# Optimization experiments

Hardware: AMD Instinct MI355X
Metric: run time of the kernel (lower is better)

Reference implementation:

```python
import jax, jax.numpy as jnp
import numpy as np

N_CLASSES = 80
SCORE_THRESH = 0.3
NMS_THRESH = 0.3
TOPK = 100            # max candidates kept per (image, class) for fixed-shape NMS
MAX_PER_IMAGE = 50
ANCHORS = np.array([[10,13],[16,30],[33,23],[30,61],[62,45],[59,119],
                    [116,90],[156,198],[373,326]], dtype=np.float32)
ANCHOR_MASK = ((6,7,8),(3,4,5),(0,1,2))


def setup_inputs() -> dict:
    key = jax.random.key(0)
    k0, k1, k2 = jax.random.split(key, 3)
    B = 16
    feat0 = jax.random.normal(k0, (B, 255, 19, 19), jnp.float32)
    feat1 = jax.random.normal(k1, (B, 255, 38, 38), jnp.float32)
    feat2 = jax.random.normal(k2, (B, 255, 76, 76), jnp.float32)
    anchors = jnp.asarray(ANCHORS)
    image_shape = jnp.array([480.0, 640.0], jnp.float32)  # (h, w) of original image
    return {"feat0": feat0, "feat1": feat1, "feat2": feat2,
            "anchors": anchors, "image_shape": image_shape}


def _decode_scale(feat, anchors_s, input_hw, image_shape):
    # feat: [B, 3*(5+C), gh, gw] -> boxes [B, gh*gw*3, 4], scores [B, gh*gw*3, C]
    B, _, gh, gw = feat.shape
    fm = feat.reshape(B, 3, 5 + N_CLASSES, gh, gw).transpose(0, 3, 4, 1, 2)  # [B,gh,gw,3,5+C]
    gy, gx = jnp.meshgrid(jnp.arange(gh, dtype=feat.dtype),
                          jnp.arange(gw, dtype=feat.dtype), indexing='ij')
    grid = jnp.stack([gx, gy], -1)[None, :, :, None, :]           # [1,gh,gw,1,2] (x,y)
    box_xy = (jax.nn.sigmoid(fm[..., :2]) + grid) / jnp.array([gh, gw], feat.dtype)
    box_wh = anchors_s[None, None, None, :, :] * jnp.exp(fm[..., 2:4]) / input_hw
    conf = jax.nn.sigmoid(fm[..., 4:5])
    probs = jax.nn.sigmoid(fm[..., 5:])
    # letterbox correction (keras-yolo3 yolo_correct_boxes)
    box_yx = box_xy[..., ::-1]
    box_hw = box_wh[..., ::-1]
    new_shape = jnp.round(image_shape * jnp.min(input_hw / image_shape))
    offset = (input_hw - new_shape) / 2.0 / input_hw
    scale = input_hw / new_shape
    box_yx = (box_yx - offset) * scale
    box_hw = box_hw * scale
    mins = box_yx - box_hw / 2.0
    maxes = box_yx + box_hw / 2.0
    boxes = jnp.concatenate([mins, maxes], -1) * jnp.concatenate([image_shape, image_shape])
    scores = conf * probs
    return boxes.reshape(B, -1, 4), scores.reshape(B, -1, N_CLASSES)


def _iou_matrix(b):  # b: [K,4] as (y1,x1,y2,x2)
    y1, x1, y2, x2 = b[:, 0], b[:, 1], b[:, 2], b[:, 3]
    area = (y2 - y1) * (x2 - x1)
    iy1 = jnp.maximum(y1[:, None], y1[None, :])
    ix1 = jnp.maximum(x1[:, None], x1[None, :])
    iy2 = jnp.minimum(y2[:, None], y2[None, :])
    ix2 = jnp.minimum(x2[:, None], x2[None, :])
    inter = jnp.maximum(iy2 - iy1, 0.0) * jnp.maximum(ix2 - ix1, 0.0)
    return inter / (area[:, None] + area[None, :] - inter + 1e-9)


def _nms_class(boxes, scores):  # boxes [N,4], scores [N] -> dets [TOPK,5] (zero-padded)
    s = jnp.where(scores > SCORE_THRESH, scores, -1.0)
    top_s, idx = jax.lax.top_k(s, TOPK)      # candidates sorted descending
    b = boxes[idx]                            # [TOPK,4]
    iou = _iou_matrix(b)
    valid = top_s > SCORE_THRESH
    ar = jnp.arange(TOPK)
    def body(i, keep):
        active = keep[i] & valid[i]
        sup = active & (iou[i] > NMS_THRESH) & (ar > i)
        return keep & ~sup
    keep = jax.lax.fori_loop(0, TOPK, body, valid)
    dets = jnp.concatenate([b, top_s[:, None]], -1)
    return dets * keep[:, None].astype(b.dtype)


def reference(feat0, feat1, feat2, anchors, image_shape):
    input_hw = jnp.array([feat0.shape[2] * 32, feat0.shape[3] * 32], feat0.dtype)
    boxes_all, scores_all = [], []
    for feat, mask in zip((feat0, feat1, feat2), ANCHOR_MASK):
        bx, sc = _decode_scale(feat, anchors[jnp.array(mask)], input_hw, image_shape)
        boxes_all.append(bx)
        scores_all.append(sc)
    boxes = jnp.concatenate(boxes_all, 1)    # [B,N,4]
    scores = jnp.concatenate(scores_all, 1)  # [B,N,C]
    nms_bc = jax.vmap(jax.vmap(_nms_class, in_axes=(None, 0)), in_axes=(0, 0))
    dets = nms_bc(boxes, scores.transpose(0, 2, 1))  # [B,C,TOPK,5]
    def cap(d):  # keep only top MAX_PER_IMAGE detections per image (by score)
        s = d[..., 4].reshape(-1)
        _, ix = jax.lax.top_k(s, MAX_PER_IMAGE)
        m = jnp.zeros(s.shape, bool).at[ix].set(True)
        return d * m.reshape(N_CLASSES, TOPK, 1).astype(d.dtype)
    return jax.vmap(cap)(dets)
```

## Files before the change

kernel.cpp:

```cpp
#include <hip/hip_runtime.h>
#include <math.h>

#define BATCH 16
#define NCLS 80
#define TOPK 100
#define NBOX 22743
#define NSLOT (NCLS*TOPK)
#define TPAD 22752
#define CAP 1024
#define NQ4 5688
#define NSEG 18
#define NCHK 4
#define WCHK 356
#define NZERO (BATCH*NCLS*256 + BATCH*NCLS)

__device__ __forceinline__ float sigf(float x){ return 1.0f/(1.0f + expf(-x)); }
__device__ __forceinline__ float fsigf(float x){
    return __builtin_amdgcn_rcpf(1.0f + __expf(-x));
}

#define BIN_OF(sc) ({ int _b = (int)(__float_as_uint(sc)>>16) - 0x3E99; _b < 0 ? 0 : (_b > 255 ? 255 : _b); })

struct Seg { const float* fbase; int a; int P; int qc; int confb; int nb; int lqoff; int tailq; };
__device__ __forceinline__ Seg segdec(int z, const float* f0, const float* f1, const float* f2){
    Seg s;
    if (z < 3){       s.a=z;   s.P=361;  s.qc=91;  s.confb=z*364;                s.nb=z;        s.fbase=f0; s.lqoff=0;      s.tailq=90; }
    else if (z < 6){  int a=z-3; s.a=a;  s.P=1444; s.qc=361; s.confb=1092+a*1444; s.nb=1083+a;  s.fbase=f1; s.lqoff=0;      s.tailq=-1; }
    else { int t=z-6; int a=t>>2, ch=t&3; s.a=a; s.P=5776; s.qc=361;
           s.confb=5424+a*5776+ch*1444;  s.nb=5415+a;  s.fbase=f2; s.lqoff=ch*361; s.tailq=-1; }
    return s;
}

struct QGeo { int s; int a; int p; int P; int conf_off; int nb; bool tail; };
__device__ __forceinline__ QGeo qgeo(int i){
    QGeo g;
    if (i < 273){        g.s=0; g.a=i/91;   int lq=i-g.a*91;   g.P=361;  g.conf_off=g.a*364      + lq*4; g.nb=g.a;      g.p=lq*4; g.tail=(lq==90); }
    else if (i < 1356){  int l=i-273;  g.s=1; g.a=l/361;  int lq=l-g.a*361;  g.P=1444; g.conf_off=1092+g.a*1444+ lq*4; g.nb=1083+g.a; g.p=lq*4; g.tail=false; }
    else {               int l=i-1356; g.s=2; g.a=l/1444; int lq=l-g.a*1444; g.P=5776; g.conf_off=5424+g.a*5776+ lq*4; g.nb=5415+g.a; g.p=lq*4; g.tail=false; }
    return g;
}

__global__ __launch_bounds__(256)
void decode_kernel(const float* __restrict__ f0, const float* __restrict__ f1,
                   const float* __restrict__ f2, const float* __restrict__ anchors,
                   const float* __restrict__ ishape,
                   float* __restrict__ boxes, float* __restrict__ conf2,
                   unsigned* __restrict__ gzero)
{
    int i = blockIdx.x*256 + threadIdx.x;
    int b = blockIdx.y;
    int tot = gridDim.x*gridDim.y*256;
    for (int g = (b*gridDim.x + blockIdx.x)*256 + threadIdx.x; g < NZERO; g += tot)
        gzero[g] = 0u;
    if (i >= NQ4) return;
    QGeo g = qgeo(i);
    const float* f = (g.s==0)?f0:((g.s==1)?f1:f2);
    int G = (g.s==0)?19:((g.s==1)?38:76);
    int abase = (g.s==0)?6:((g.s==1)?3:0);
    const float* fb = f + ((size_t)b*255 + g.a*85)*(size_t)g.P;
    float4 TX = *(const float4*)(fb + (size_t)0*g.P + g.p);
    float4 TY = *(const float4*)(fb + (size_t)1*g.P + g.p);
    float4 TW = *(const float4*)(fb + (size_t)2*g.P + g.p);
    float4 TH = *(const float4*)(fb + (size_t)3*g.P + g.p);
    float4 TC = *(const float4*)(fb + (size_t)4*g.P + g.p);
    const float* txp = (const float*)&TX; const float* typ = (const float*)&TY;
    const float* twp = (const float*)&TW; const float* thp = (const float*)&TH;
    const float* tcp = (const float*)&TC;

    float aw = anchors[(abase+g.a)*2+0];
    float ah = anchors[(abase+g.a)*2+1];
    float ih = ishape[0], iw = ishape[1];
    float mm = fminf(608.0f/ih, 608.0f/iw);
    float nh = rintf(ih*mm), nw = rintf(iw*mm);
    float offy = (608.0f - nh) / 2.0f / 608.0f;
    float offx = (608.0f - nw) / 2.0f / 608.0f;
    float scy = 608.0f/nh, scx = 608.0f/nw;
    float gg = (float)G;
    int valid = g.tail ? 1 : 4;
    float cfout[4] = {0.f, 0.f, 0.f, 0.f};
#pragma unroll
    for (int j=0; j<4; j++){
        if (j < valid){
            int px = g.p + j;
            int yy = px / G, xx = px - yy*G;
            float xn = (sigf(txp[j]) + (float)xx) / gg;
            float yn = (sigf(typ[j]) + (float)yy) / gg;
            float wn = aw * expf(twp[j]) / 608.0f;
            float hn = ah * expf(thp[j]) / 608.0f;
            float y = (yn - offy)*scy;
            float x = (xn - offx)*scx;
            float hh = hn*scy, ww = wn*scx;
            int n = g.nb + 3*px;
            float4 bx;
            bx.x = (y - hh/2.0f)*ih;
            bx.y = (x - ww/2.0f)*iw;
            bx.z = (y + hh/2.0f)*ih;
            bx.w = (x + ww/2.0f)*iw;
            *(float4*)&boxes[((size_t)b*NBOX + n)*4] = bx;
            cfout[j] = sigf(tcp[j]);
        }
    }
    float4 cv; cv.x=cfout[0]; cv.y=cfout[1]; cv.z=cfout[2]; cv.w=cfout[3];
    *(float4*)&conf2[(size_t)b*TPAD + g.conf_off] = cv;
}

template<bool WRITEB>
__global__ __launch_bounds__(256)
void scan_kernel(const float* __restrict__ f0, const float* __restrict__ f1,
                 const float* __restrict__ f2, const float* __restrict__ conf2,
                 unsigned int* __restrict__ ghist, unsigned char* __restrict__ binb)
{
    int cg = blockIdx.x, b = blockIdx.y, z = blockIdx.z, tid = threadIdx.x;
    int c0 = cg*4;
    int bc0 = b*NCLS + c0;
    __shared__ unsigned int h[4][256];
    h[0][tid]=0; h[1][tid]=0; h[2][tid]=0; h[3][tid]=0;
    __syncthreads();
    Seg sg = segdec(z, f0, f1, f2);
    const int P = sg.P, qc = sg.qc;
    const float* cfp = conf2 + (size_t)b*TPAD + sg.confb;
    const float* prb = sg.fbase + ((size_t)b*255 + sg.a*85 + 5 + c0)*(size_t)P + sg.lqoff*4;

    int lqA = tid, lqB = tid + 256;
    bool vA = lqA < qc, vB = lqB < qc;
    float4 cfA, cfB, A0, A1, A2, A3, B0, B1, B2, B3;
    if (vA){
        const float* pA = prb + lqA*4;
        cfA = *(const float4*)(cfp + lqA*4);
        A0 = *(const float4*)pA;         A1 = *(const float4*)(pA + P);
        A2 = *(const float4*)(pA + 2*P); A3 = *(const float4*)(pA + 3*P);
    }
    if (vB){
        const float* pB = prb + lqB*4;
        cfB = *(const float4*)(cfp + lqB*4);
        B0 = *(const float4*)pB;         B1 = *(const float4*)(pB + P);
        B2 = *(const float4*)(pB + 2*P); B3 = *(const float4*)(pB + 3*P);
    }
#define HQUAD(cls, Q, CF, LQ) { \
    float s0 = CF.x*fsigf(Q.x), s1 = CF.y*fsigf(Q.y), s2 = CF.z*fsigf(Q.z), s3 = CF.w*fsigf(Q.w); \
    int b0 = BIN_OF(s0), b1 = BIN_OF(s1), b2 = BIN_OF(s2), b3 = BIN_OF(s3); \
    bool k0 = s0 > 0.2995f, k1 = s1 > 0.2995f, k2 = s2 > 0.2995f, k3 = s3 > 0.2995f; \
    if (k0) atomicAdd(&h[cls][b0], 1u); \
    if (k1) atomicAdd(&h[cls][b1], 1u); \
    if (k2) atomicAdd(&h[cls][b2], 1u); \
    if (k3) atomicAdd(&h[cls][b3], 1u); \
    if (WRITEB){ \
        unsigned ub = (k0 ? (unsigned)(b0+1) : 0u) | ((k1 ? (unsigned)(b1+1) : 0u)<<8) \
                    | ((k2 ? (unsigned)(b2+1) : 0u)<<16) | ((k3 ? (unsigned)(b3+1) : 0u)<<24); \
        *(unsigned*)(binb + (size_t)(bc0+cls)*TPAD + sg.confb + (LQ)*4) = ub; } }
    if (vA){
        if (lqA == sg.tailq){
            A0.y=A0.z=A0.w=-INFINITY; A1.y=A1.z=A1.w=-INFINITY;
            A2.y=A2.z=A2.w=-INFINITY; A3.y=A3.z=A3.w=-INFINITY;
        }
        HQUAD(0, A0, cfA, lqA) HQUAD(1, A1, cfA, lqA) HQUAD(2, A2, cfA, lqA) HQUAD(3, A3, cfA, lqA)
    }
    if (vB){
        HQUAD(0, B0, cfB, lqB) HQUAD(1, B1, cfB, lqB) HQUAD(2, B2, cfB, lqB) HQUAD(3, B3, cfB, lqB)
    }
#undef HQUAD
    __syncthreads();
    size_t hb = ((size_t)bc0)*256 + tid;
    if (h[0][tid]) atomicAdd(&ghist[hb      ], h[0][tid]);
    if (h[1][tid]) atomicAdd(&ghist[hb + 256], h[1][tid]);
    if (h[2][tid]) atomicAdd(&ghist[hb + 512], h[2][tid]);
    if (h[3][tid]) atomicAdd(&ghist[hb + 768], h[3][tid]);
}

template<bool WITHB>
__global__ __launch_bounds__(256)
void compact3_kernel(const float* __restrict__ f0, const float* __restrict__ f1,
                     const float* __restrict__ f2, const float* __restrict__ conf2,
                     const unsigned char* __restrict__ binb,
                     const unsigned int* __restrict__ ghist,
                     int* __restrict__ gcnt, float* __restrict__ gsc,
                     int* __restrict__ gix)
{
    int c = blockIdx.x, b = blockIdx.y, z = blockIdx.z, tid = threadIdx.x;
    int bc = b*NCLS + c;
    __shared__ int sufA[256], sufB[256];
    __shared__ int TbS;
    if (tid == 0) TbS = 0;
    sufA[tid] = (int)ghist[(size_t)bc*256 + tid];
    __syncthreads();
    int* cur = sufA; int* nxt = sufB;
    for (int d=1; d<256; d<<=1){
        int v = cur[tid] + ((tid+d) < 256 ? cur[tid+d] : 0);
        nxt[tid] = v;
        __syncthreads();
        int* t_ = cur; cur = nxt; nxt = t_;
    }
    if (cur[tid] >= TOPK && (tid == 255 || cur[tid+1] < TOPK)) TbS = tid;
    __syncthreads();
    int gate = TbS - 2; if (gate < 0) gate = 0;

    if (WITHB){
        const uint4* bw = (const uint4*)(binb + (size_t)bc*TPAD);
        int ibeg = z*WCHK, iend = (z+1)*WCHK;
        if (iend > NQ4/4) iend = NQ4/4;
        for (int i = ibeg + tid; i < iend; i += 256){
            uint4 u4 = bw[i];
            unsigned wv[4] = {u4.x, u4.y, u4.z, u4.w};
#pragma unroll
            for (int k=0; k<4; k++){
                unsigned ub = wv[k];
                if (!ub) continue;
                int w = i*4 + k;
                QGeo g = qgeo(w);
                const float* f = (g.s==0)?f0:((g.s==1)?f1:f2);
                const float* pr = f + ((size_t)b*255 + g.a*85 + 5 + c)*(size_t)g.P + g.p;
#pragma unroll
                for (int j=0; j<4; j++){
                    unsigned bj = (ub >> (8*j)) & 0xFFu;
                    if (bj && (int)bj - 1 >= gate){
                        float cf = conf2[(size_t)b*TPAD + w*4 + j];
                        float pv = pr[j];
                        float sc = cf * sigf(pv);
                        int pos = atomicAdd(&gcnt[bc], 1);
                        if (pos < CAP){
                            gsc[(size_t)bc*CAP + pos] = sc;
                            gix[(size_t)bc*CAP + pos] = g.nb + 3*(g.p + j);
                        }
                    }
                }
            }
        }
    } else {
        int qbeg = z*(NQ4/NCHK + 1), qend = qbeg + (NQ4/NCHK + 1);
        if (qend > NQ4) qend = NQ4;
        for (int i = qbeg + tid; i < qend; i += 256){
            QGeo g = qgeo(i);
            const float* f = (g.s==0)?f0:((g.s==1)?f1:f2);
            float4 cf4 = *(const float4*)(conf2 + (size_t)b*TPAD + g.conf_off);
            const float* pr = f + ((size_t)b*255 + g.a*85 + 5 + c)*(size_t)g.P + g.p;
            float pv[4];
            if (!g.tail){
                float4 t = *(const float4*)pr;
                pv[0]=t.x; pv[1]=t.y; pv[2]=t.z; pv[3]=t.w;
            } else {
                pv[0] = pr[0]; pv[1] = -INFINITY; pv[2] = -INFINITY; pv[3] = -INFINITY;
            }
            const float* cfp = (const float*)&cf4;
#pragma unroll
            for (int j=0; j<4; j++){
                float st = cfp[j]*fsigf(pv[j]);
                if (st > 0.2995f && BIN_OF(st) >= gate){
                    float sc = cfp[j]*sigf(pv[j]);
                    int pos = atomicAdd(&gcnt[bc], 1);
                    if (pos < CAP){
                        gsc[(size_t)bc*CAP + pos] = sc;
                        gix[(size_t)bc*CAP + pos] = g.nb + 3*(g.p + j);
                    }
                }
            }
        }
    }
}

__global__ __launch_bounds__(256)
void sortnms2_kernel(const float* __restrict__ gsc, const int* __restrict__ gix,
                     const int* __restrict__ gcnt, const float* __restrict__ boxes,
                     float* __restrict__ out)
{
    int c = blockIdx.x, b = blockIdx.y, tid = threadIdx.x;
    int bc = b*NCLS + c;
    __shared__ float cs[CAP];
    __shared__ int   ci[CAP];
    __shared__ float by1[TOPK], bx1[TOPK], by2[TOPK], bx2[TOPK], bar_[TOPK];
    __shared__ unsigned sup[TOPK][4];
    __shared__ unsigned keepw[4];
    int n = gcnt[bc]; if (n > CAP) n = CAP;
    for (int t=tid; t<CAP; t+=256){
        if (t < n){ cs[t] = gsc[(size_t)bc*CAP + t]; ci[t] = gix[(size_t)bc*CAP + t]; }
        else { cs[t] = -INFINITY; ci[t] = 0x7FFFFFFF; }
    }
    if (tid < 4) keepw[tid] = 0u;
    for (int r=tid; r<TOPK; r+=256){ sup[r][0]=0u; sup[r][1]=0u; sup[r][2]=0u; sup[r][3]=0u; }
    __syncthreads();
    int S = 128; while (S < n) S <<= 1;
    for (int k=2; k<=S; k<<=1){
        for (int j=k>>1; j>0; j>>=1){
            for (int t=tid; t<S; t+=256){
                int ixj = t ^ j;
                if (ixj > t){
                    float s1 = cs[t], s2 = cs[ixj];
                    int   i1 = ci[t], i2 = ci[ixj];
                    bool b2_first = (s2 > s1) || (s2 == s1 && i2 < i1);
                    bool b1_first = (s1 > s2) || (s1 == s2 && i1 < i2);
                    bool desc = ((t & k) == 0);
                    bool sw = desc ? b2_first : b1_first;
                    if (sw){ cs[t]=s2; cs[ixj]=s1; ci[t]=i2; ci[ixj]=i1; }
                }
            }
            __syncthreads();
        }
    }

    if (tid < TOPK){
        float s = cs[tid];
        float y1=0.f,x1=0.f,y2=0.f,x2=0.f;
        if (s > 0.3f){
            size_t q = ((size_t)b*NBOX + ci[tid])*4;
            y1=boxes[q]; x1=boxes[q+1]; y2=boxes[q+2]; x2=boxes[q+3];
            atomicOr(&keepw[tid>>5], 1u << (tid & 31));
        }
        by1[tid]=y1; bx1[tid]=x1; by2[tid]=y2; bx2[tid]=x2;
        bar_[tid] = (y2-y1)*(x2-x1);
    }
    __syncthreads();

    for (int p = tid; p < TOPK*TOPK; p += 256){
        int i = p / TOPK, j = p - i*TOPK;
        if (j > i){
            float q1 = fmaxf(by1[i], by1[j]);
            float q2 = fmaxf(bx1[i], bx1[j]);
            float q3 = fminf(by2[i], by2[j]);
            float q4 = fminf(bx2[i], bx2[j]);
            float inter = fmaxf(q3-q1, 0.0f)*fmaxf(q4-q2, 0.0f);
            float iou = inter/(bar_[i] + bar_[j] - inter + 1e-9f);
            if (iou > 0.3f) atomicOr(&sup[i][j>>5], 1u << (j & 31));
        }
    }
    __syncthreads();

    if (tid == 0){
        unsigned k0 = keepw[0], k1 = keepw[1], k2 = keepw[2], k3 = keepw[3];
        for (int i = 0; i < TOPK; i++){
            uint4 sp = *(const uint4*)sup[i];
            unsigned kw = (i < 32) ? k0 : ((i < 64) ? k1 : ((i < 96) ? k2 : k3));
            if (kw & (1u << (i & 31))){
                k0 &= ~sp.x; k1 &= ~sp.y; k2 &= ~sp.z; k3 &= ~sp.w;
            }
        }
        keepw[0]=k0; keepw[1]=k1; keepw[2]=k2; keepw[3]=k3;
    }
    __syncthreads();

    if (tid < TOPK){
        bool kept = (keepw[tid>>5] >> (tid & 31)) & 1u;
        size_t o5 = ((size_t)(bc*TOPK + tid))*5;
        out[o5+0] = kept ? by1[tid] : 0.f;
        out[o5+1] = kept ? bx1[tid] : 0.f;
        out[o5+2] = kept ? by2[tid] : 0.f;
        out[o5+3] = kept ? bx2[tid] : 0.f;
        out[o5+4] = kept ? cs[tid]  : 0.f;
    }
}

__global__ __launch_bounds__(1024)
void cap_kernel(float* __restrict__ out)
{
    int b = blockIdx.x, tid = threadIdx.x;
    __shared__ unsigned int h[256];
    __shared__ int sufA[256], sufB[256];
    __shared__ float cs[512];
    __shared__ int   ci[512];
    __shared__ int cnt, T50;
    __shared__ unsigned char msk[NSLOT];
    if (tid < 256) h[tid] = 0;
    if (tid == 0){ cnt = 0; T50 = 0; }
    for (int u=tid; u<NSLOT; u+=1024) msk[u] = 0;
    __syncthreads();

    for (int u=tid; u<NSLOT; u+=1024){
        float v = out[((size_t)b*NSLOT + u)*5 + 4];
        if (v > 0.0f) atomicAdd(&h[BIN_OF(v)], 1u);
    }
    __syncthreads();

    if (tid < 256) sufA[tid] = (int)h[tid];
    __syncthreads();
    int* cur = sufA; int* nxt = sufB;
    for (int d=1; d<256; d<<=1){
        if (tid < 256) nxt[tid] = cur[tid] + ((tid+d) < 256 ? cur[tid+d] : 0);
        __syncthreads();
        int* t_ = cur; cur = nxt; nxt = t_;
    }
    if (tid < 256){
        if (cur[tid] >= 50 && (tid == 255 || cur[tid+1] < 50)) T50 = tid;
    }
    __syncthreads();
    int T = T50;

    for (int u=tid; u<NSLOT; u+=1024){
        float v = out[((size_t)b*NSLOT + u)*5 + 4];
        if (v > 0.0f && BIN_OF(v) >= T){
            int pos = atomicAdd(&cnt, 1);
            if (pos < 512){ cs[pos] = v; ci[pos] = u; }
        }
    }
    __syncthreads();
    int n = cnt; if (n > 512) n = 512;
    for (int t=tid; t<512; t+=1024){
        if (t >= n){ cs[t] = -INFINITY; ci[t] = 0x7FFFFFFF; }
    }
    __syncthreads();

    int S = 64; while (S < n) S <<= 1;
    for (int k=2; k<=S; k<<=1){
        for (int j=k>>1; j>0; j>>=1){
            for (int t=tid; t<S; t+=1024){
                int ixj = t ^ j;
                if (ixj > t){
                    float s1 = cs[t], s2 = cs[ixj];
                    int   i1 = ci[t], i2 = ci[ixj];
                    bool b2_first = (s2 > s1) || (s2 == s1 && i2 < i1);
                    bool b1_first = (s1 > s2) || (s1 == s2 && i1 < i2);
                    bool desc = ((t & k) == 0);
                    bool sw = desc ? b2_first : b1_first;
                    if (sw){ cs[t]=s2; cs[ixj]=s1; ci[t]=i2; ci[ixj]=i1; }
                }
            }
            __syncthreads();
        }
    }

    if (tid < 50 && tid < n) msk[ci[tid]] = 1;
    __syncthreads();

    for (int u=tid; u<NSLOT; u+=1024){
        size_t o5 = ((size_t)b*NSLOT + u)*5;
        float v = out[o5 + 4];
        if (v > 0.0f && !msk[u]){
            out[o5+0]=0.f; out[o5+1]=0.f; out[o5+2]=0.f; out[o5+3]=0.f; out[o5+4]=0.f;
        }
    }
}

extern "C" void kernel_launch(void* const* d_in, const int* in_sizes, int n_in,
                              void* d_out, int out_size, void* d_ws, size_t ws_size,
                              hipStream_t stream)
{
    const float* f0 = (const float*)d_in[0];
    const float* f1 = (const float*)d_in[1];
    const float* f2 = (const float*)d_in[2];
    const float* anchors = (const float*)d_in[3];
    const float* ishape  = (const float*)d_in[4];
    float* out = (float*)d_out;

    float* boxes = (float*)d_ws;
    float* conf2 = boxes + (size_t)BATCH*NBOX*4;
    unsigned* ghist = (unsigned*)(conf2 + (size_t)BATCH*TPAD);
    int* gcnt = (int*)(ghist + (size_t)BATCH*NCLS*256);
    float* gsc = (float*)(gcnt + BATCH*NCLS);
    int*   gix = (int*)(gsc + (size_t)BATCH*NCLS*CAP);
    unsigned char* binb = (unsigned char*)(gix + (size_t)BATCH*NCLS*CAP);

    size_t words = (size_t)BATCH*NBOX*4 + (size_t)BATCH*TPAD + (size_t)NZERO
                 + 2*(size_t)BATCH*NCLS*CAP;
    size_t need = words*4 + (size_t)BATCH*NCLS*TPAD;
    bool useB = ws_size >= need;

    dim3 dgrid((NQ4 + 255)/256, BATCH);
    decode_kernel<<<dgrid, 256, 0, stream>>>(f0, f1, f2, anchors, ishape,
                                             boxes, conf2, ghist);

    dim3 hgrid(NCLS/4, BATCH, NSEG);
    if (useB)
        scan_kernel<true><<<hgrid, 256, 0, stream>>>(f0, f1, f2, conf2, ghist, binb);
    else
        scan_kernel<false><<<hgrid, 256, 0, stream>>>(f0, f1, f2, conf2, ghist, binb);

    dim3 cgrid(NCLS, BATCH, NCHK);
    if (useB)
        compact3_kernel<true><<<cgrid, 256, 0, stream>>>(f0, f1, f2, conf2, binb,
                                                         ghist, gcnt, gsc, gix);
    else
        compact3_kernel<false><<<cgrid, 256, 0, stream>>>(f0, f1, f2, conf2, binb,
                                                          ghist, gcnt, gsc, gix);

    dim3 sgrid(NCLS, BATCH);
    sortnms2_kernel<<<sgrid, 256, 0, stream>>>(gsc, gix, gcnt, boxes, out);

    cap_kernel<<<BATCH, 1024, 0, stream>>>(out);
}
```

Measured before the change: 137.1 us.

## Fuse candidate compaction into sort/NMS kernel using shared-memory buffers

Merges the compaction kernel and the sort/NMS kernel into one per-(image,class) block. Selected candidates are appended to shared memory through a shared atomic counter instead of a global counter and global score/index arrays. This removes a kernel launch, the global round trip for candidates, and the zeroing of the global counters. In exchange, the per-block scan over the bin bytes is no longer split across 4 z-chunks, so each block does more serial work and the grid has less parallelism.

```diff
diff --git a/kernel.cpp b/kernel.cpp
--- a/kernel.cpp
+++ b/kernel.cpp
@@ -10,9 +10,7 @@
 #define CAP 1024
 #define NQ4 5688
 #define NSEG 18
-#define NCHK 4
-#define WCHK 356
-#define NZERO (BATCH*NCLS*256 + BATCH*NCLS)
+#define NZERO (BATCH*NCLS*256)
 
 __device__ __forceinline__ float sigf(float x){ return 1.0f/(1.0f + expf(-x)); }
 __device__ __forceinline__ float fsigf(float x){
@@ -169,18 +167,24 @@
 
 template<bool WITHB>
 __global__ __launch_bounds__(256)
-void compact3_kernel(const float* __restrict__ f0, const float* __restrict__ f1,
-                     const float* __restrict__ f2, const float* __restrict__ conf2,
-                     const unsigned char* __restrict__ binb,
-                     const unsigned int* __restrict__ ghist,
-                     int* __restrict__ gcnt, float* __restrict__ gsc,
-                     int* __restrict__ gix)
+void selnms_kernel(const float* __restrict__ f0, const float* __restrict__ f1,
+                   const float* __restrict__ f2, const float* __restrict__ conf2,
+                   const unsigned char* __restrict__ binb,
+                   const unsigned int* __restrict__ ghist,
+                   const float* __restrict__ boxes, float* __restrict__ out)
 {
-    int c = blockIdx.x, b = blockIdx.y, z = blockIdx.z, tid = threadIdx.x;
+    int c = blockIdx.x, b = blockIdx.y, tid = threadIdx.x;
     int bc = b*NCLS + c;
     __shared__ int sufA[256], sufB[256];
-    __shared__ int TbS;
-    if (tid == 0) TbS = 0;
+    __shared__ float cs[CAP];
+    __shared__ int   ci[CAP];
+    __shared__ float by1[TOPK], bx1[TOPK], by2[TOPK], bx2[TOPK], bar_[TOPK];
+    __shared__ unsigned sup[TOPK][4];
+    __shared__ unsigned keepw[4];
+    __shared__ int cnt, TbS;
+    if (tid == 0){ cnt = 0; TbS = 0; }
+    if (tid < 4) keepw[tid] = 0u;
+    for (int r=tid; r<TOPK; r+=256){ sup[r][0]=0u; sup[r][1]=0u; sup[r][2]=0u; sup[r][3]=0u; }
     sufA[tid] = (int)ghist[(size_t)bc*256 + tid];
     __syncthreads();
     int* cur = sufA; int* nxt = sufB;
@@ -196,9 +200,7 @@
 
     if (WITHB){
         const uint4* bw = (const uint4*)(binb + (size_t)bc*TPAD);
-        int ibeg = z*WCHK, iend = (z+1)*WCHK;
-        if (iend > NQ4/4) iend = NQ4/4;
-        for (int i = ibeg + tid; i < iend; i += 256){
+        for (int i = tid; i < NQ4/4; i += 256){
             uint4 u4 = bw[i];
             unsigned wv[4] = {u4.x, u4.y, u4.z, u4.w};
 #pragma unroll
@@ -216,19 +218,14 @@
                         float cf = conf2[(size_t)b*TPAD + w*4 + j];
                         float pv = pr[j];
                         float sc = cf * sigf(pv);
-                        int pos = atomicAdd(&gcnt[bc], 1);
-                        if (pos < CAP){
-                            gsc[(size_t)bc*CAP + pos] = sc;
-                            gix[(size_t)bc*CAP + pos] = g.nb + 3*(g.p + j);
-                        }
+                        int pos = atomicAdd(&cnt, 1);
+                        if (pos < CAP){ cs[pos] = sc; ci[pos] = g.nb + 3*(g.p + j); }
                     }
                 }
             }
         }
     } else {
-        int qbeg = z*(NQ4/NCHK + 1), qend = qbeg + (NQ4/NCHK + 1);
-        if (qend > NQ4) qend = NQ4;
-        for (int i = qbeg + tid; i < qend; i += 256){
+        for (int i = tid; i < NQ4; i += 256){
             QGeo g = qgeo(i);
             const float* f = (g.s==0)?f0:((g.s==1)?f1:f2);
             float4 cf4 = *(const float4*)(conf2 + (size_t)b*TPAD + g.conf_off);
@@ -246,38 +243,20 @@
                 float st = cfp[j]*fsigf(pv[j]);
                 if (st > 0.2995f && BIN_OF(st) >= gate){
                     float sc = cfp[j]*sigf(pv[j]);
-                    int pos = atomicAdd(&gcnt[bc], 1);
-                    if (pos < CAP){
-                        gsc[(size_t)bc*CAP + pos] = sc;
-                        gix[(size_t)bc*CAP + pos] = g.nb + 3*(g.p + j);
-                    }
+                    int pos = atomicAdd(&cnt, 1);
+                    if (pos < CAP){ cs[pos] = sc; ci[pos] = g.nb + 3*(g.p + j); }
                 }
             }
         }
     }
-}
-
-__global__ __launch_bounds__(256)
-void sortnms2_kernel(const float* __restrict__ gsc, const int* __restrict__ gix,
-                     const int* __restrict__ gcnt, const float* __restrict__ boxes,
-                     float* __restrict__ out)
-{
-    int c = blockIdx.x, b = blockIdx.y, tid = threadIdx.x;
-    int bc = b*NCLS + c;
-    __shared__ float cs[CAP];
-    __shared__ int   ci[CAP];
-    __shared__ float by1[TOPK], bx1[TOPK], by2[TOPK], bx2[TOPK], bar_[TOPK];
-    __shared__ unsigned sup[TOPK][4];
-    __shared__ unsigned keepw[4];
-    int n = gcnt[bc]; if (n > CAP) n = CAP;
-    for (int t=tid; t<CAP; t+=256){
-        if (t < n){ cs[t] = gsc[(size_t)bc*CAP + t]; ci[t] = gix[(size_t)bc*CAP + t]; }
-        else { cs[t] = -INFINITY; ci[t] = 0x7FFFFFFF; }
-    }
-    if (tid < 4) keepw[tid] = 0u;
-    for (int r=tid; r<TOPK; r+=256){ sup[r][0]=0u; sup[r][1]=0u; sup[r][2]=0u; sup[r][3]=0u; }
-    __syncthreads();
+    __syncthreads();
+    int n = cnt; if (n > CAP) n = CAP;
+
     int S = 128; while (S < n) S <<= 1;
+    for (int t=tid; t<S; t+=256){
+        if (t >= n){ cs[t] = -INFINITY; ci[t] = 0x7FFFFFFF; }
+    }
+    __syncthreads();
     for (int k=2; k<=S; k<<=1){
         for (int j=k>>1; j>0; j>>=1){
             for (int t=tid; t<S; t+=256){
@@ -441,13 +420,9 @@
     float* boxes = (float*)d_ws;
     float* conf2 = boxes + (size_t)BATCH*NBOX*4;
     unsigned* ghist = (unsigned*)(conf2 + (size_t)BATCH*TPAD);
-    int* gcnt = (int*)(ghist + (size_t)BATCH*NCLS*256);
-    float* gsc = (float*)(gcnt + BATCH*NCLS);
-    int*   gix = (int*)(gsc + (size_t)BATCH*NCLS*CAP);
-    unsigned char* binb = (unsigned char*)(gix + (size_t)BATCH*NCLS*CAP);
-
-    size_t words = (size_t)BATCH*NBOX*4 + (size_t)BATCH*TPAD + (size_t)NZERO
-                 + 2*(size_t)BATCH*NCLS*CAP;
+    unsigned char* binb = (unsigned char*)(ghist + (size_t)NZERO);
+
+    size_t words = (size_t)BATCH*NBOX*4 + (size_t)BATCH*TPAD + (size_t)NZERO;
     size_t need = words*4 + (size_t)BATCH*NCLS*TPAD;
     bool useB = ws_size >= need;
 
@@ -461,16 +436,13 @@
     else
         scan_kernel<false><<<hgrid, 256, 0, stream>>>(f0, f1, f2, conf2, ghist, binb);
 
-    dim3 cgrid(NCLS, BATCH, NCHK);
+    dim3 sgrid(NCLS, BATCH);
     if (useB)
-        compact3_kernel<true><<<cgrid, 256, 0, stream>>>(f0, f1, f2, conf2, binb,
-                                                         ghist, gcnt, gsc, gix);
+        selnms_kernel<true><<<sgrid, 256, 0, stream>>>(f0, f1, f2, conf2, binb,
+                                                       ghist, boxes, out);
     else
-        compact3_kernel<false><<<cgrid, 256, 0, stream>>>(f0, f1, f2, conf2, binb,
-                                                          ghist, gcnt, gsc, gix);
-
-    dim3 sgrid(NCLS, BATCH);
-    sortnms2_kernel<<<sgrid, 256, 0, stream>>>(gsc, gix, gcnt, boxes, out);
+        selnms_kernel<false><<<sgrid, 256, 0, stream>>>(f0, f1, f2, conf2, binb,
+                                                        ghist, boxes, out);
 
     cap_kernel<<<BATCH, 1024, 0, stream>>>(out);
 }
```

After: 114.6 us, median of 2. 16.4% less time.
